# Performance work log

Measured on AMD Instinct MI355X. Metric: run time of the kernel, lower is better.

The kernel has to match this reference:

```python
import jax, jax.numpy as jnp
import numpy as np

SIM_THRESHOLD = 0.9


def setup_inputs() -> dict:
    key = jax.random.key(0)
    k1, k2 = jax.random.split(key)
    # patches: b * c * num * ws * ws  (b=2, c=8, num=1024, ws=3) -> n = 16384
    patches = jax.random.normal(k1, (2, 8, 1024, 3, 3), dtype=jnp.float32)
    # db: m * ws * ws
    db = jax.random.normal(k2, (16384, 3, 3), dtype=jnp.float32)
    return {"patches": patches, "db": db}


def reference(patches, db):
    ws = patches.shape[-1]
    p = patches.reshape(-1, ws, ws)          # [n, ws, ws]
    n = p.shape[0]
    m = db.shape[0]
    pf = p.reshape(n, -1)                    # [n, ws*ws]
    df = db.reshape(m, -1)                   # [m, ws*ws]
    dot = pf @ df.T                          # [n, m], tiny K=ws*ws -> memory bound
    norm_n = jnp.linalg.norm(pf, axis=1, keepdims=True)   # [n, 1]
    norm_m = jnp.linalg.norm(df, axis=1, keepdims=True)   # [m, 1]
    cos = dot / (norm_n * norm_m.T)          # [n, m] cosine similarity
    # patch kept only if dissimilar to EVERY db entry
    mask = jnp.all(cos < SIM_THRESHOLD, axis=1)            # [n] bool
    # jit-friendly fixed-shape compaction: zero out rejected patches instead of
    # dropping rows (original does db = cat(db, patches[mask]))
    filtered = jnp.where(mask[:, None, None], p, jnp.zeros((), p.dtype))
    return jnp.concatenate([db.reshape(-1, ws, ws), filtered], axis=0)  # [m+n, ws, ws]
```

## Files before the change

### kernel.cpp

```cpp
#include <hip/hip_runtime.h>

#define NPATCH 16384
#define NDB    16384
#define WS9    9
#define KP     16
#define JCH    32
#define CHUNK  (NDB / JCH)
#define TILES  (CHUNK / 32)
#define BAND_LO 0.89998f
#define BAND_HI 0.90002f
#define PREP_BLOCKS 144

typedef short bf16x8 __attribute__((ext_vector_type(8)));
typedef float f32x16 __attribute__((ext_vector_type(16)));

#define MAX3(a,b,c) fmaxf(fmaxf((a),(b)),(c))

__device__ __forceinline__ float np_norm9(const float* v) {
#pragma clang fp contract(off)
    float q0 = v[0] * v[0], q1 = v[1] * v[1], q2 = v[2] * v[2], q3 = v[3] * v[3];
    float q4 = v[4] * v[4], q5 = v[5] * v[5], q6 = v[6] * v[6], q7 = v[7] * v[7];
    float q8 = v[8] * v[8];
    float s = ((q0 + q1) + (q2 + q3)) + ((q4 + q5) + (q6 + q7));
    s = s + q8;
    return sqrtf(s);
}

__device__ __forceinline__ unsigned short f2bf(float x) {
    unsigned u = __float_as_uint(x);
    return (unsigned short)((u + 0x7fffu + ((u >> 16) & 1u)) >> 16);
}
__device__ __forceinline__ float bf2f(unsigned short h) {
    return __uint_as_float(((unsigned)h) << 16);
}

__device__ __forceinline__ void stage_row(const float* __restrict__ src,
                                          unsigned short* dh, unsigned short* dl) {
    float v[WS9];
#pragma unroll
    for (int k = 0; k < WS9; k++) v[k] = src[k];
    float inv = 1.0f / np_norm9(v);
    unsigned short h[KP], l[KP];
#pragma unroll
    for (int k = 0; k < KP; k++) {
        float x = (k < WS9) ? v[k] * inv : 0.0f;
        h[k] = f2bf(x);
        l[k] = f2bf(x - bf2f(h[k]));
    }
    int hw[8], lw[8];
#pragma unroll
    for (int k = 0; k < 8; k++) {
        hw[k] = (int)h[2 * k] | ((int)h[2 * k + 1] << 16);
        lw[k] = (int)l[2 * k] | ((int)l[2 * k + 1] << 16);
    }
    ((int4*)dh)[0] = make_int4(hw[0], hw[1], hw[2], hw[3]);
    ((int4*)dh)[1] = make_int4(hw[4], hw[5], hw[6], hw[7]);
    ((int4*)dl)[0] = make_int4(lw[0], lw[1], lw[2], lw[3]);
    ((int4*)dl)[1] = make_int4(lw[4], lw[5], lw[6], lw[7]);
}

__global__ __launch_bounds__(256) void k_prep(const float* __restrict__ patches,
                                              const float* __restrict__ db,
                                              unsigned short* __restrict__ pnh,
                                              unsigned short* __restrict__ pnl,
                                              unsigned short* __restrict__ dnh,
                                              unsigned short* __restrict__ dnl,
                                              float* __restrict__ out,
                                              int* __restrict__ band_count) {
    int t = blockIdx.x * 256 + threadIdx.x;
    if (t == 0) *band_count = 0;
    ((float4*)out)[t] = ((const float4*)db)[t];
    if (t < NPATCH) {
        stage_row(patches + (size_t)t * WS9, &pnh[(size_t)t * KP], &pnl[(size_t)t * KP]);
    } else if (t < 2 * NPATCH) {
        int r = t - NPATCH;
        stage_row(db + (size_t)r * WS9, &dnh[(size_t)r * KP], &dnl[(size_t)r * KP]);
    }
}

__global__ __launch_bounds__(256) void k_phase1(const unsigned short* __restrict__ pnh,
                                                const unsigned short* __restrict__ pnl,
                                                const unsigned short* __restrict__ dnh,
                                                const unsigned short* __restrict__ dnl,
                                                float* __restrict__ partial) {
    __shared__ __align__(16) unsigned short s_dh[CHUNK * KP];
    __shared__ __align__(16) unsigned short s_dl[CHUNK * KP];

    int jbase = blockIdx.y * CHUNK;
    int ibase = blockIdx.x * 256;

    {
        const int4* gh = (const int4*)(dnh + (size_t)jbase * KP);
        const int4* gl = (const int4*)(dnl + (size_t)jbase * KP);
        int4* sh = (int4*)s_dh;
        int4* sl = (int4*)s_dl;
#pragma unroll
        for (int u = 0; u < 4; u++) {
            int e = u * 256 + threadIdx.x;
            sh[e] = gh[e];
            sl[e] = gl[e];
        }
    }

    int lane = threadIdx.x & 63;
    int wave = threadIdx.x >> 6;
    int col = lane & 31;
    int half = lane >> 5;
    int i0 = ibase + wave * 64;

    const bf16x8* Ph = (const bf16x8*)pnh;
    const bf16x8* Pl = (const bf16x8*)pnl;
    bf16x8 b_hi0 = Ph[(size_t)(i0 + col) * 2 + half];
    bf16x8 b_lo0 = Pl[(size_t)(i0 + col) * 2 + half];
    bf16x8 b_hi1 = Ph[(size_t)(i0 + 32 + col) * 2 + half];
    bf16x8 b_lo1 = Pl[(size_t)(i0 + 32 + col) * 2 + half];

    __syncthreads();

    const bf16x8* Ah = (const bf16x8*)s_dh;
    const bf16x8* Al = (const bf16x8*)s_dl;

    f32x16 zc = {0.f,0.f,0.f,0.f,0.f,0.f,0.f,0.f,0.f,0.f,0.f,0.f,0.f,0.f,0.f,0.f};
    float rm0 = -3.0e38f, rm1 = -3.0e38f;

#pragma unroll 2
    for (int t = 0; t < TILES; ++t) {
        bf16x8 a_h = Ah[(t * 32 + col) * 2 + half];
        bf16x8 a_l = Al[(t * 32 + col) * 2 + half];
        f32x16 acc0 = __builtin_amdgcn_mfma_f32_32x32x16_bf16(a_h, b_hi0, zc, 0, 0, 0);
        acc0 = __builtin_amdgcn_mfma_f32_32x32x16_bf16(a_h, b_lo0, acc0, 0, 0, 0);
        acc0 = __builtin_amdgcn_mfma_f32_32x32x16_bf16(a_l, b_hi0, acc0, 0, 0, 0);
        f32x16 acc1 = __builtin_amdgcn_mfma_f32_32x32x16_bf16(a_h, b_hi1, zc, 0, 0, 0);
        acc1 = __builtin_amdgcn_mfma_f32_32x32x16_bf16(a_h, b_lo1, acc1, 0, 0, 0);
        acc1 = __builtin_amdgcn_mfma_f32_32x32x16_bf16(a_l, b_hi1, acc1, 0, 0, 0);
        {
            float u0 = MAX3(acc0[0],  acc0[1],  acc0[2]);
            float u1 = MAX3(acc0[3],  acc0[4],  acc0[5]);
            float u2 = MAX3(acc0[6],  acc0[7],  acc0[8]);
            float u3 = MAX3(acc0[9],  acc0[10], acc0[11]);
            float u4 = MAX3(acc0[12], acc0[13], acc0[14]);
            float u5 = MAX3(u0, u1, acc0[15]);
            float u6 = MAX3(u2, u3, u4);
            rm0 = MAX3(u5, u6, rm0);
        }
        {
            float u0 = MAX3(acc1[0],  acc1[1],  acc1[2]);
            float u1 = MAX3(acc1[3],  acc1[4],  acc1[5]);
            float u2 = MAX3(acc1[6],  acc1[7],  acc1[8]);
            float u3 = MAX3(acc1[9],  acc1[10], acc1[11]);
            float u4 = MAX3(acc1[12], acc1[13], acc1[14]);
            float u5 = MAX3(u0, u1, acc1[15]);
            float u6 = MAX3(u2, u3, u4);
            rm1 = MAX3(u5, u6, rm1);
        }
    }
    rm0 = fmaxf(rm0, __shfl_xor(rm0, 32, 64));
    rm1 = fmaxf(rm1, __shfl_xor(rm1, 32, 64));
    int ti = half ? (i0 + 32 + col) : (i0 + col);
    partial[(size_t)blockIdx.y * NPATCH + ti] = half ? rm1 : rm0;
}

__global__ __launch_bounds__(256) void k_classify(const float* __restrict__ patches,
                                                  const float* __restrict__ partial,
                                                  float* __restrict__ out,
                                                  int* __restrict__ band_list,
                                                  int* __restrict__ band_count) {
    int i = blockIdx.x * 256 + threadIdx.x;
    float cosmax = partial[i];
#pragma unroll
    for (int c = 1; c < JCH; c++)
        cosmax = fmaxf(cosmax, partial[(size_t)c * NPATCH + i]);
    if (cosmax >= BAND_LO && cosmax < BAND_HI) {
        int idx = atomicAdd(band_count, 1);
        band_list[idx] = i;
        return;
    }
    int hit = (cosmax >= BAND_HI) ? 1 : 0;
#pragma unroll
    for (int k = 0; k < WS9; k++)
        out[(size_t)(NDB + i) * WS9 + k] = hit ? 0.0f : patches[(size_t)i * WS9 + k];
}

__global__ __launch_bounds__(256) void k_phase2(const float* __restrict__ patches,
                                                const float* __restrict__ db,
                                                const int* __restrict__ band_list,
                                                const int* __restrict__ band_count,
                                                float* __restrict__ out) {
    __shared__ float sp[WS9];
    __shared__ float snp;
    __shared__ int shit;
    int nb = *band_count;
    for (int idx = blockIdx.x; idx < nb; idx += gridDim.x) {
        int i = band_list[idx];
        if (threadIdx.x == 0) {
            float p[WS9];
            for (int k = 0; k < WS9; k++) { p[k] = patches[(size_t)i * WS9 + k]; sp[k] = p[k]; }
            snp = np_norm9(p);
            shit = 0;
        }
        __syncthreads();
        float p[WS9];
#pragma unroll
        for (int k = 0; k < WS9; k++) p[k] = sp[k];
        float npn = snp;
        int hit = 0;
        for (int j = (int)threadIdx.x; j < NDB; j += 256) {
            float d[WS9];
#pragma unroll
            for (int k = 0; k < WS9; k++) d[k] = db[(size_t)j * WS9 + k];
            float dot = 0.0f;
#pragma unroll
            for (int k = 0; k < WS9; k++) dot = fmaf(p[k], d[k], dot);
            float nd = np_norm9(d);
            float cs = dot / (npn * nd);
            if (!((double)cs < 0.9)) hit = 1;
        }
        if (hit) atomicOr(&shit, 1);
        __syncthreads();
        int m = shit;
        if (threadIdx.x < WS9)
            out[(size_t)(NDB + i) * WS9 + threadIdx.x] = m ? 0.0f : sp[threadIdx.x];
        __syncthreads();
    }
}

extern "C" void kernel_launch(void* const* d_in, const int* in_sizes, int n_in,
                              void* d_out, int out_size, void* d_ws, size_t ws_size,
                              hipStream_t stream) {
    const float* patches = (const float*)d_in[0];
    const float* db      = (const float*)d_in[1];
    float* out = (float*)d_out;

    char* wsb = (char*)d_ws;
    size_t o_partial = 0;
    size_t o_blist   = (size_t)JCH * NPATCH * 4;
    size_t o_bcount  = o_blist + (size_t)NPATCH * 4;
    size_t o_pnh     = o_bcount + 256;
    size_t o_pnl     = o_pnh + (size_t)NPATCH * KP * 2;
    size_t o_dnh     = o_pnl + (size_t)NPATCH * KP * 2;
    size_t o_dnl     = o_dnh + (size_t)NDB * KP * 2;

    float* partial          = (float*)(wsb + o_partial);
    int*   band_list        = (int*)(wsb + o_blist);
    int*   band_count       = (int*)(wsb + o_bcount);
    unsigned short* pnh     = (unsigned short*)(wsb + o_pnh);
    unsigned short* pnl     = (unsigned short*)(wsb + o_pnl);
    unsigned short* dnh     = (unsigned short*)(wsb + o_dnh);
    unsigned short* dnl     = (unsigned short*)(wsb + o_dnl);

    k_prep<<<dim3(PREP_BLOCKS), dim3(256), 0, stream>>>(patches, db, pnh, pnl,
                                                        dnh, dnl, out, band_count);
    k_phase1<<<dim3(NPATCH / 256, JCH), dim3(256), 0, stream>>>(pnh, pnl, dnh, dnl,
                                                                partial);
    k_classify<<<dim3(NPATCH / 256), dim3(256), 0, stream>>>(patches, partial, out,
                                                             band_list, band_count);
    k_phase2<<<dim3(256), dim3(256), 0, stream>>>(patches, db, band_list, band_count, out);
}
```

Before: 101.5 us.

## Fuse phase1, classify and phase2 into one kernel via atomic max and last-block completion

The per-chunk max cosine is now reduced with an atomicMax on an order-preserving integer key instead of being written to a partial buffer. A per-row-block counter elects the last finishing block, which then classifies its 256 patches and runs the exact fp32 recheck for borderline ones. This drops two kernel launches and the partial-buffer round trip. In exchange it adds global atomics, and the exact rechecks are now serialized inside whichever block finishes last rather than spread across 256 blocks.

```diff
diff --git a/kernel.cpp b/kernel.cpp
--- a/kernel.cpp
+++ b/kernel.cpp
@@ -34,6 +34,14 @@
     return __uint_as_float(((unsigned)h) << 16);
 }
 
+__device__ __forceinline__ int enc_key(float f) {
+    int k = __float_as_int(f);
+    return (k >= 0) ? k : (k ^ 0x7FFFFFFF);
+}
+__device__ __forceinline__ float dec_key(int k) {
+    return __int_as_float((k >= 0) ? k : (k ^ 0x7FFFFFFF));
+}
+
 __device__ __forceinline__ void stage_row(const float* __restrict__ src,
                                           unsigned short* dh, unsigned short* dl) {
     float v[WS9];
@@ -66,41 +74,40 @@
                                               unsigned short* __restrict__ dnh,
                                               unsigned short* __restrict__ dnl,
                                               float* __restrict__ out,
-                                              int* __restrict__ band_count) {
+                                              int* __restrict__ cosk,
+                                              int* __restrict__ done) {
     int t = blockIdx.x * 256 + threadIdx.x;
-    if (t == 0) *band_count = 0;
     ((float4*)out)[t] = ((const float4*)db)[t];
     if (t < NPATCH) {
+        cosk[t] = (int)0x80000000;
         stage_row(patches + (size_t)t * WS9, &pnh[(size_t)t * KP], &pnl[(size_t)t * KP]);
     } else if (t < 2 * NPATCH) {
         int r = t - NPATCH;
         stage_row(db + (size_t)r * WS9, &dnh[(size_t)r * KP], &dnl[(size_t)r * KP]);
     }
-}
-
-__global__ __launch_bounds__(256) void k_phase1(const unsigned short* __restrict__ pnh,
-                                                const unsigned short* __restrict__ pnl,
-                                                const unsigned short* __restrict__ dnh,
-                                                const unsigned short* __restrict__ dnl,
-                                                float* __restrict__ partial) {
+    if (t < NPATCH / 256) done[t] = 0;
+}
+
+__global__ __launch_bounds__(256) void k_main(const unsigned short* __restrict__ pnh,
+                                              const unsigned short* __restrict__ pnl,
+                                              const unsigned short* __restrict__ dnh,
+                                              const unsigned short* __restrict__ dnl,
+                                              const float* __restrict__ patches,
+                                              const float* __restrict__ db,
+                                              float* __restrict__ out,
+                                              int* __restrict__ cosk,
+                                              int* __restrict__ done) {
     __shared__ __align__(16) unsigned short s_dh[CHUNK * KP];
     __shared__ __align__(16) unsigned short s_dl[CHUNK * KP];
+    __shared__ int s_old;
+    __shared__ int s_bn;
+    __shared__ int s_blist[256];
+    __shared__ float sp[WS9];
+    __shared__ float snp;
+    __shared__ int shit;
 
     int jbase = blockIdx.y * CHUNK;
     int ibase = blockIdx.x * 256;
-
-    {
-        const int4* gh = (const int4*)(dnh + (size_t)jbase * KP);
-        const int4* gl = (const int4*)(dnl + (size_t)jbase * KP);
-        int4* sh = (int4*)s_dh;
-        int4* sl = (int4*)s_dl;
-#pragma unroll
-        for (int u = 0; u < 4; u++) {
-            int e = u * 256 + threadIdx.x;
-            sh[e] = gh[e];
-            sl[e] = gl[e];
-        }
-    }
 
     int lane = threadIdx.x & 63;
     int wave = threadIdx.x >> 6;
@@ -115,6 +122,18 @@
     bf16x8 b_hi1 = Ph[(size_t)(i0 + 32 + col) * 2 + half];
     bf16x8 b_lo1 = Pl[(size_t)(i0 + 32 + col) * 2 + half];
 
+    {
+        const int4* gh = (const int4*)(dnh + (size_t)jbase * KP);
+        const int4* gl = (const int4*)(dnl + (size_t)jbase * KP);
+        int4* sh = (int4*)s_dh;
+        int4* sl = (int4*)s_dl;
+#pragma unroll
+        for (int u = 0; u < 4; u++) {
+            int e = u * 256 + threadIdx.x;
+            sh[e] = gh[e];
+            sl[e] = gl[e];
+        }
+    }
     __syncthreads();
 
     const bf16x8* Ah = (const bf16x8*)s_dh;
@@ -157,44 +176,37 @@
     rm0 = fmaxf(rm0, __shfl_xor(rm0, 32, 64));
     rm1 = fmaxf(rm1, __shfl_xor(rm1, 32, 64));
     int ti = half ? (i0 + 32 + col) : (i0 + col);
-    partial[(size_t)blockIdx.y * NPATCH + ti] = half ? rm1 : rm0;
-}
-
-__global__ __launch_bounds__(256) void k_classify(const float* __restrict__ patches,
-                                                  const float* __restrict__ partial,
-                                                  float* __restrict__ out,
-                                                  int* __restrict__ band_list,
-                                                  int* __restrict__ band_count) {
-    int i = blockIdx.x * 256 + threadIdx.x;
-    float cosmax = partial[i];
-#pragma unroll
-    for (int c = 1; c < JCH; c++)
-        cosmax = fmaxf(cosmax, partial[(size_t)c * NPATCH + i]);
+    atomicMax(&cosk[ti], enc_key(half ? rm1 : rm0));
+
+    __syncthreads();
+    if (threadIdx.x == 0) {
+        s_old = __hip_atomic_fetch_add(&done[blockIdx.x], 1,
+                                       __ATOMIC_ACQ_REL, __HIP_MEMORY_SCOPE_AGENT);
+        s_bn = 0;
+    }
+    __syncthreads();
+    if (s_old != JCH - 1) return;
+
+    int i = ibase + threadIdx.x;
+    int key = __hip_atomic_load(&cosk[i], __ATOMIC_ACQUIRE, __HIP_MEMORY_SCOPE_AGENT);
+    float cosmax = dec_key(key);
     if (cosmax >= BAND_LO && cosmax < BAND_HI) {
-        int idx = atomicAdd(band_count, 1);
-        band_list[idx] = i;
-        return;
-    }
-    int hit = (cosmax >= BAND_HI) ? 1 : 0;
-#pragma unroll
-    for (int k = 0; k < WS9; k++)
-        out[(size_t)(NDB + i) * WS9 + k] = hit ? 0.0f : patches[(size_t)i * WS9 + k];
-}
-
-__global__ __launch_bounds__(256) void k_phase2(const float* __restrict__ patches,
-                                                const float* __restrict__ db,
-                                                const int* __restrict__ band_list,
-                                                const int* __restrict__ band_count,
-                                                float* __restrict__ out) {
-    __shared__ float sp[WS9];
-    __shared__ float snp;
-    __shared__ int shit;
-    int nb = *band_count;
-    for (int idx = blockIdx.x; idx < nb; idx += gridDim.x) {
-        int i = band_list[idx];
+        int idx = atomicAdd(&s_bn, 1);
+        s_blist[idx] = i;
+    } else {
+        int hit = (cosmax >= BAND_HI) ? 1 : 0;
+#pragma unroll
+        for (int k = 0; k < WS9; k++)
+            out[(size_t)(NDB + i) * WS9 + k] = hit ? 0.0f : patches[(size_t)i * WS9 + k];
+    }
+    __syncthreads();
+    int nb = s_bn;
+
+    for (int e = 0; e < nb; e++) {
+        int bi = s_blist[e];
         if (threadIdx.x == 0) {
             float p[WS9];
-            for (int k = 0; k < WS9; k++) { p[k] = patches[(size_t)i * WS9 + k]; sp[k] = p[k]; }
+            for (int k = 0; k < WS9; k++) { p[k] = patches[(size_t)bi * WS9 + k]; sp[k] = p[k]; }
             snp = np_norm9(p);
             shit = 0;
         }
@@ -219,7 +231,7 @@
         __syncthreads();
         int m = shit;
         if (threadIdx.x < WS9)
-            out[(size_t)(NDB + i) * WS9 + threadIdx.x] = m ? 0.0f : sp[threadIdx.x];
+            out[(size_t)(NDB + bi) * WS9 + threadIdx.x] = m ? 0.0f : sp[threadIdx.x];
         __syncthreads();
     }
 }
@@ -232,27 +244,23 @@
     float* out = (float*)d_out;
 
     char* wsb = (char*)d_ws;
-    size_t o_partial = 0;
-    size_t o_blist   = (size_t)JCH * NPATCH * 4;
-    size_t o_bcount  = o_blist + (size_t)NPATCH * 4;
-    size_t o_pnh     = o_bcount + 256;
-    size_t o_pnl     = o_pnh + (size_t)NPATCH * KP * 2;
-    size_t o_dnh     = o_pnl + (size_t)NPATCH * KP * 2;
-    size_t o_dnl     = o_dnh + (size_t)NDB * KP * 2;
-
-    float* partial          = (float*)(wsb + o_partial);
-    int*   band_list        = (int*)(wsb + o_blist);
-    int*   band_count       = (int*)(wsb + o_bcount);
-    unsigned short* pnh     = (unsigned short*)(wsb + o_pnh);
-    unsigned short* pnl     = (unsigned short*)(wsb + o_pnl);
-    unsigned short* dnh     = (unsigned short*)(wsb + o_dnh);
-    unsigned short* dnl     = (unsigned short*)(wsb + o_dnl);
+    size_t o_cosk = 0;
+    size_t o_done = (size_t)NPATCH * 4;
+    size_t o_pnh  = o_done + 256;
+    size_t o_pnl  = o_pnh + (size_t)NPATCH * KP * 2;
+    size_t o_dnh  = o_pnl + (size_t)NPATCH * KP * 2;
+    size_t o_dnl  = o_dnh + (size_t)NDB * KP * 2;
+
+    int* cosk           = (int*)(wsb + o_cosk);
+    int* done           = (int*)(wsb + o_done);
+    unsigned short* pnh = (unsigned short*)(wsb + o_pnh);
+    unsigned short* pnl = (unsigned short*)(wsb + o_pnl);
+    unsigned short* dnh = (unsigned short*)(wsb + o_dnh);
+    unsigned short* dnl = (unsigned short*)(wsb + o_dnl);
 
     k_prep<<<dim3(PREP_BLOCKS), dim3(256), 0, stream>>>(patches, db, pnh, pnl,
-                                                        dnh, dnl, out, band_count);
-    k_phase1<<<dim3(NPATCH / 256, JCH), dim3(256), 0, stream>>>(pnh, pnl, dnh, dnl,
-                                                                partial);
-    k_classify<<<dim3(NPATCH / 256), dim3(256), 0, stream>>>(patches, partial, out,
-                                                             band_list, band_count);
-    k_phase2<<<dim3(256), dim3(256), 0, stream>>>(patches, db, band_list, band_count, out);
-}
+                                                        dnh, dnl, out, cosk, done);
+    k_main<<<dim3(NPATCH / 256, JCH), dim3(256), 0, stream>>>(pnh, pnl, dnh, dnl,
+                                                              patches, db, out,
+                                                              cosk, done);
+}
```

Measured after the change: 119.6 us. 1.18x slower.

## Read db tiles directly from global with register prefetch, drop LDS staging

Applied to the files above, without the earlier changes.

The dot kernel no longer stages each db chunk into shared memory behind a barrier. It loads the bf16 hi/lo tiles straight from global (L2-cached) into registers, software-pipelined two tiles ahead. The db split drops from 32 to 16 slices, so each block covers twice as many rows and the finish kernel reduces fewer partials. The prefetch reads up to two tiles past each slice, which the padding added to the workspace layout is meant to keep in bounds, at the cost of more global load traffic per wave and fewer blocks overall.

```diff
diff --git a/kernel.cpp b/kernel.cpp
--- a/kernel.cpp
+++ b/kernel.cpp
@@ -4,11 +4,12 @@
 #define NDB    16384
 #define WS9    9
 #define KP     16
-#define JCH    32
-#define CHUNK  (NDB / JCH)
-#define TILES  (CHUNK / 32)
+#define GSL    16
+#define SLROWS (NDB / GSL)
+#define NT     (SLROWS / 32)
 #define BAND_LO 0.89998f
 #define BAND_HI 0.90002f
+#define COPY_BLOCKS 144
 #define PREP_BLOCKS 144
 
 typedef short bf16x8 __attribute__((ext_vector_type(8)));
@@ -78,62 +79,45 @@
     }
 }
 
-__global__ __launch_bounds__(256) void k_phase1(const unsigned short* __restrict__ pnh,
-                                                const unsigned short* __restrict__ pnl,
-                                                const unsigned short* __restrict__ dnh,
-                                                const unsigned short* __restrict__ dnl,
-                                                float* __restrict__ partial) {
-    __shared__ __align__(16) unsigned short s_dh[CHUNK * KP];
-    __shared__ __align__(16) unsigned short s_dl[CHUNK * KP];
-
-    int jbase = blockIdx.y * CHUNK;
-    int ibase = blockIdx.x * 256;
-
-    {
-        const int4* gh = (const int4*)(dnh + (size_t)jbase * KP);
-        const int4* gl = (const int4*)(dnl + (size_t)jbase * KP);
-        int4* sh = (int4*)s_dh;
-        int4* sl = (int4*)s_dl;
-#pragma unroll
-        for (int u = 0; u < 4; u++) {
-            int e = u * 256 + threadIdx.x;
-            sh[e] = gh[e];
-            sl[e] = gl[e];
-        }
-    }
-
+__global__ __launch_bounds__(256) void k_dot(const unsigned short* __restrict__ pnh,
+                                             const unsigned short* __restrict__ pnl,
+                                             const unsigned short* __restrict__ dnh,
+                                             const unsigned short* __restrict__ dnl,
+                                             float* __restrict__ partial) {
     int lane = threadIdx.x & 63;
     int wave = threadIdx.x >> 6;
     int col = lane & 31;
     int half = lane >> 5;
-    int i0 = ibase + wave * 64;
+    int i0 = blockIdx.x * 256 + wave * 64;
+    int rowbase = blockIdx.y * SLROWS;
 
     const bf16x8* Ph = (const bf16x8*)pnh;
     const bf16x8* Pl = (const bf16x8*)pnl;
-    bf16x8 b_hi0 = Ph[(size_t)(i0 + col) * 2 + half];
-    bf16x8 b_lo0 = Pl[(size_t)(i0 + col) * 2 + half];
-    bf16x8 b_hi1 = Ph[(size_t)(i0 + 32 + col) * 2 + half];
-    bf16x8 b_lo1 = Pl[(size_t)(i0 + 32 + col) * 2 + half];
-
-    __syncthreads();
-
-    const bf16x8* Ah = (const bf16x8*)s_dh;
-    const bf16x8* Al = (const bf16x8*)s_dl;
+    bf16x8 b_hi0 = Ph[(i0 + col) * 2 + half];
+    bf16x8 b_lo0 = Pl[(i0 + col) * 2 + half];
+    bf16x8 b_hi1 = Ph[(i0 + 32 + col) * 2 + half];
+    bf16x8 b_lo1 = Pl[(i0 + 32 + col) * 2 + half];
+
+    const bf16x8* Ah = (const bf16x8*)dnh;
+    const bf16x8* Al = (const bf16x8*)dnl;
+#define AH(tt) Ah[(rowbase + (tt) * 32 + col) * 2 + half]
+#define AL(tt) Al[(rowbase + (tt) * 32 + col) * 2 + half]
 
     f32x16 zc = {0.f,0.f,0.f,0.f,0.f,0.f,0.f,0.f,0.f,0.f,0.f,0.f,0.f,0.f,0.f,0.f};
     float rm0 = -3.0e38f, rm1 = -3.0e38f;
 
-#pragma unroll 2
-    for (int t = 0; t < TILES; ++t) {
-        bf16x8 a_h = Ah[(t * 32 + col) * 2 + half];
-        bf16x8 a_l = Al[(t * 32 + col) * 2 + half];
-        f32x16 acc0 = __builtin_amdgcn_mfma_f32_32x32x16_bf16(a_h, b_hi0, zc, 0, 0, 0);
-        acc0 = __builtin_amdgcn_mfma_f32_32x32x16_bf16(a_h, b_lo0, acc0, 0, 0, 0);
-        acc0 = __builtin_amdgcn_mfma_f32_32x32x16_bf16(a_l, b_hi0, acc0, 0, 0, 0);
-        f32x16 acc1 = __builtin_amdgcn_mfma_f32_32x32x16_bf16(a_h, b_hi1, zc, 0, 0, 0);
-        acc1 = __builtin_amdgcn_mfma_f32_32x32x16_bf16(a_h, b_lo1, acc1, 0, 0, 0);
-        acc1 = __builtin_amdgcn_mfma_f32_32x32x16_bf16(a_l, b_hi1, acc1, 0, 0, 0);
+    bf16x8 ah0 = AH(0), al0 = AL(0);
+    bf16x8 ah1 = AH(1), al1 = AL(1);
+
+    for (int tt = 0; tt < NT; tt += 2) {
+        bf16x8 nh0 = AH(tt + 2), nl0 = AL(tt + 2);
         {
+            f32x16 acc0 = __builtin_amdgcn_mfma_f32_32x32x16_bf16(ah0, b_hi0, zc, 0, 0, 0);
+            acc0 = __builtin_amdgcn_mfma_f32_32x32x16_bf16(ah0, b_lo0, acc0, 0, 0, 0);
+            acc0 = __builtin_amdgcn_mfma_f32_32x32x16_bf16(al0, b_hi0, acc0, 0, 0, 0);
+            f32x16 acc1 = __builtin_amdgcn_mfma_f32_32x32x16_bf16(ah0, b_hi1, zc, 0, 0, 0);
+            acc1 = __builtin_amdgcn_mfma_f32_32x32x16_bf16(ah0, b_lo1, acc1, 0, 0, 0);
+            acc1 = __builtin_amdgcn_mfma_f32_32x32x16_bf16(al0, b_hi1, acc1, 0, 0, 0);
             float u0 = MAX3(acc0[0],  acc0[1],  acc0[2]);
             float u1 = MAX3(acc0[3],  acc0[4],  acc0[5]);
             float u2 = MAX3(acc0[6],  acc0[7],  acc0[8]);
@@ -142,33 +126,59 @@
             float u5 = MAX3(u0, u1, acc0[15]);
             float u6 = MAX3(u2, u3, u4);
             rm0 = MAX3(u5, u6, rm0);
-        }
+            float w0 = MAX3(acc1[0],  acc1[1],  acc1[2]);
+            float w1 = MAX3(acc1[3],  acc1[4],  acc1[5]);
+            float w2 = MAX3(acc1[6],  acc1[7],  acc1[8]);
+            float w3 = MAX3(acc1[9],  acc1[10], acc1[11]);
+            float w4 = MAX3(acc1[12], acc1[13], acc1[14]);
+            float w5 = MAX3(w0, w1, acc1[15]);
+            float w6 = MAX3(w2, w3, w4);
+            rm1 = MAX3(w5, w6, rm1);
+        }
+        bf16x8 nh1 = AH(tt + 3), nl1 = AL(tt + 3);
         {
-            float u0 = MAX3(acc1[0],  acc1[1],  acc1[2]);
-            float u1 = MAX3(acc1[3],  acc1[4],  acc1[5]);
-            float u2 = MAX3(acc1[6],  acc1[7],  acc1[8]);
-            float u3 = MAX3(acc1[9],  acc1[10], acc1[11]);
-            float u4 = MAX3(acc1[12], acc1[13], acc1[14]);
-            float u5 = MAX3(u0, u1, acc1[15]);
+            f32x16 acc0 = __builtin_amdgcn_mfma_f32_32x32x16_bf16(ah1, b_hi0, zc, 0, 0, 0);
+            acc0 = __builtin_amdgcn_mfma_f32_32x32x16_bf16(ah1, b_lo0, acc0, 0, 0, 0);
+            acc0 = __builtin_amdgcn_mfma_f32_32x32x16_bf16(al1, b_hi0, acc0, 0, 0, 0);
+            f32x16 acc1 = __builtin_amdgcn_mfma_f32_32x32x16_bf16(ah1, b_hi1, zc, 0, 0, 0);
+            acc1 = __builtin_amdgcn_mfma_f32_32x32x16_bf16(ah1, b_lo1, acc1, 0, 0, 0);
+            acc1 = __builtin_amdgcn_mfma_f32_32x32x16_bf16(al1, b_hi1, acc1, 0, 0, 0);
+            float u0 = MAX3(acc0[0],  acc0[1],  acc0[2]);
+            float u1 = MAX3(acc0[3],  acc0[4],  acc0[5]);
+            float u2 = MAX3(acc0[6],  acc0[7],  acc0[8]);
+            float u3 = MAX3(acc0[9],  acc0[10], acc0[11]);
+            float u4 = MAX3(acc0[12], acc0[13], acc0[14]);
+            float u5 = MAX3(u0, u1, acc0[15]);
             float u6 = MAX3(u2, u3, u4);
-            rm1 = MAX3(u5, u6, rm1);
-        }
-    }
+            rm0 = MAX3(u5, u6, rm0);
+            float w0 = MAX3(acc1[0],  acc1[1],  acc1[2]);
+            float w1 = MAX3(acc1[3],  acc1[4],  acc1[5]);
+            float w2 = MAX3(acc1[6],  acc1[7],  acc1[8]);
+            float w3 = MAX3(acc1[9],  acc1[10], acc1[11]);
+            float w4 = MAX3(acc1[12], acc1[13], acc1[14]);
+            float w5 = MAX3(w0, w1, acc1[15]);
+            float w6 = MAX3(w2, w3, w4);
+            rm1 = MAX3(w5, w6, rm1);
+        }
+        ah0 = nh0; al0 = nl0; ah1 = nh1; al1 = nl1;
+    }
+#undef AH
+#undef AL
     rm0 = fmaxf(rm0, __shfl_xor(rm0, 32, 64));
     rm1 = fmaxf(rm1, __shfl_xor(rm1, 32, 64));
     int ti = half ? (i0 + 32 + col) : (i0 + col);
     partial[(size_t)blockIdx.y * NPATCH + ti] = half ? rm1 : rm0;
 }
 
-__global__ __launch_bounds__(256) void k_classify(const float* __restrict__ patches,
-                                                  const float* __restrict__ partial,
-                                                  float* __restrict__ out,
-                                                  int* __restrict__ band_list,
-                                                  int* __restrict__ band_count) {
+__global__ __launch_bounds__(256) void k_finish(const float* __restrict__ patches,
+                                                const float* __restrict__ partial,
+                                                float* __restrict__ out,
+                                                int* __restrict__ band_list,
+                                                int* __restrict__ band_count) {
     int i = blockIdx.x * 256 + threadIdx.x;
     float cosmax = partial[i];
 #pragma unroll
-    for (int c = 1; c < JCH; c++)
+    for (int c = 1; c < GSL; c++)
         cosmax = fmaxf(cosmax, partial[(size_t)c * NPATCH + i]);
     if (cosmax >= BAND_LO && cosmax < BAND_HI) {
         int idx = atomicAdd(band_count, 1);
@@ -233,26 +243,26 @@
 
     char* wsb = (char*)d_ws;
     size_t o_partial = 0;
-    size_t o_blist   = (size_t)JCH * NPATCH * 4;
+    size_t o_blist   = (size_t)GSL * NPATCH * 4;
     size_t o_bcount  = o_blist + (size_t)NPATCH * 4;
     size_t o_pnh     = o_bcount + 256;
     size_t o_pnl     = o_pnh + (size_t)NPATCH * KP * 2;
     size_t o_dnh     = o_pnl + (size_t)NPATCH * KP * 2;
-    size_t o_dnl     = o_dnh + (size_t)NDB * KP * 2;
-
-    float* partial          = (float*)(wsb + o_partial);
-    int*   band_list        = (int*)(wsb + o_blist);
-    int*   band_count       = (int*)(wsb + o_bcount);
-    unsigned short* pnh     = (unsigned short*)(wsb + o_pnh);
-    unsigned short* pnl     = (unsigned short*)(wsb + o_pnl);
-    unsigned short* dnh     = (unsigned short*)(wsb + o_dnh);
-    unsigned short* dnl     = (unsigned short*)(wsb + o_dnl);
+    size_t o_dnl     = o_dnh + (size_t)NDB * KP * 2 + 4096;
+
+    float* partial      = (float*)(wsb + o_partial);
+    int*   band_list    = (int*)(wsb + o_blist);
+    int*   band_count   = (int*)(wsb + o_bcount);
+    unsigned short* pnh = (unsigned short*)(wsb + o_pnh);
+    unsigned short* pnl = (unsigned short*)(wsb + o_pnl);
+    unsigned short* dnh = (unsigned short*)(wsb + o_dnh);
+    unsigned short* dnl = (unsigned short*)(wsb + o_dnl);
 
     k_prep<<<dim3(PREP_BLOCKS), dim3(256), 0, stream>>>(patches, db, pnh, pnl,
                                                         dnh, dnl, out, band_count);
-    k_phase1<<<dim3(NPATCH / 256, JCH), dim3(256), 0, stream>>>(pnh, pnl, dnh, dnl,
-                                                                partial);
-    k_classify<<<dim3(NPATCH / 256), dim3(256), 0, stream>>>(patches, partial, out,
-                                                             band_list, band_count);
+    k_dot<<<dim3(NPATCH / 256, GSL), dim3(256), 0, stream>>>(pnh, pnl, dnh, dnl,
+                                                             partial);
+    k_finish<<<dim3(NPATCH / 256), dim3(256), 0, stream>>>(patches, partial, out,
+                                                           band_list, band_count);
     k_phase2<<<dim3(256), dim3(256), 0, stream>>>(patches, db, band_list, band_count, out);
 }
```

Measured after the change: 104.4 us. 1.03x slower.
